# Performance work log

Hardware: AMD Instinct MI355X
Metric: run time of the kernel (lower is better)

## Reference

```python
import jax, jax.numpy as jnp
import numpy as np

N = 50000        # nodes
E = 400000       # edges (avg degree 8)
T = 4            # edge types
D_IN = 64        # input feature dim
D_OUT = 128      # GGNN hidden / output dim
B = 64           # graphs in batch
STEPS = 8        # GRU propagation steps


def setup_inputs() -> dict:
    key = jax.random.key(0)
    ks = jax.random.split(key, 10)
    s = 1.0 / np.sqrt(D_OUT)
    features = jax.random.normal(ks[0], (N, D_IN), jnp.float32)
    src = jax.random.randint(ks[1], (E,), 0, N, jnp.int32)
    dst = jax.random.randint(ks[2], (E,), 0, N, jnp.int32)
    etype = jax.random.randint(ks[3], (E,), 0, T, jnp.int32)
    node2graph = jnp.sort(jax.random.randint(ks[4], (N,), 0, B, jnp.int32))
    # per-edge-type message Linear(out, out)
    W_msg = jax.random.normal(ks[5], (T, D_OUT, D_OUT), jnp.float32) * s
    b_msg = jnp.zeros((T, D_OUT), jnp.float32)
    # GRUCell(out, out): gate order (r, z, n) as in torch
    w_ih = jax.random.normal(ks[6], (D_OUT, 3 * D_OUT), jnp.float32) * s
    b_ih = jnp.zeros((3 * D_OUT,), jnp.float32)
    w_hh = jax.random.normal(ks[7], (D_OUT, 3 * D_OUT), jnp.float32) * s
    b_hh = jnp.zeros((3 * D_OUT,), jnp.float32)
    # classifier Linear(out, 2)
    W_cls = jax.random.normal(ks[8], (D_OUT, 2), jnp.float32) * s
    b_cls = jnp.zeros((2,), jnp.float32)
    return {"features": features, "src": src, "dst": dst, "etype": etype,
            "node2graph": node2graph, "W_msg": W_msg, "b_msg": b_msg,
            "w_ih": w_ih, "b_ih": b_ih, "w_hh": w_hh, "b_hh": b_hh,
            "W_cls": W_cls, "b_cls": b_cls}


def reference(features, src, dst, etype, node2graph, W_msg, b_msg,
              w_ih, b_ih, w_hh, b_hh, W_cls, b_cls):
    n = features.shape[0]
    # zero-pad input features to D_OUT (as in GGNN.forward)
    h1 = jnp.concatenate(
        [features, jnp.zeros((n, D_OUT - D_IN), features.dtype)], axis=-1)

    def step(h, _):
        # transform every node by every etype weight: [N, T, D]
        t = jnp.einsum('nd,tde->nte', h, W_msg) + b_msg
        msgs = t[src, etype]                       # [E, D] gather per edge
        a = jax.ops.segment_sum(msgs, dst, num_segments=n)  # scatter-sum
        # torch GRUCell(a, h), gates ordered (r, z, n)
        gi = a @ w_ih + b_ih
        gh = h @ w_hh + b_hh
        i_r, i_z, i_n = jnp.split(gi, 3, axis=-1)
        h_r, h_z, h_n = jnp.split(gh, 3, axis=-1)
        r = jax.nn.sigmoid(i_r + h_r)
        z = jax.nn.sigmoid(i_z + h_z)
        ng = jnp.tanh(i_n + r * h_n)
        return (1.0 - z) * ng + z * h, None

    h, _ = jax.lax.scan(step, h1, None, length=STEPS)
    hres = h + h1                                   # residual as in forward
    # read_out == 'sum': per-graph segment sum (dgl.sum_nodes)
    feats_g = jax.ops.segment_sum(hres, node2graph, num_segments=B)  # [B, D]
    return feats_g @ W_cls + b_cls                  # [B, 2]
```

## Files before the change

kernel.cpp:

```cpp
#include <hip/hip_runtime.h>
#include <hip/hip_bf16.h>
#include <math.h>

#define NN 50000
#define EE 400000
#define TT 4
#define DIN 64
#define DD 128
#define BB 64
#define STEPS 8
#define KAGG 544
#define KTOT 672
#define NGATES 512
#define NBIN (4 * NN)
#define NBLK ((NBIN + 255) / 256)
#define MT64 ((NN + 63) / 64)

typedef __attribute__((ext_vector_type(8))) short bf16x8;
typedef __attribute__((ext_vector_type(4))) float f32x4;
typedef __attribute__((address_space(3))) void lds_void;
typedef __attribute__((address_space(1))) void glob_void;

__device__ inline float bf2f(__hip_bfloat16 x) { return __bfloat162float(x); }

__device__ inline float s2f(short s) {
    unsigned int u = ((unsigned int)(unsigned short)s) << 16;
    float f;
    __builtin_memcpy(&f, &u, 4);
    return f;
}

__global__ void k_init_h(const float* __restrict__ feat, float* __restrict__ h1,
                         __hip_bfloat16* __restrict__ hb) {
    int idx = blockIdx.x * blockDim.x + threadIdx.x;
    if (idx >= NN * DD) return;
    int v = idx >> 7, d = idx & 127;
    float val = (d < DIN) ? feat[v * DIN + d] : 0.0f;
    h1[idx] = val;
    hb[idx] = __float2bfloat16(val);
}

__global__ void k_zero_i32(int* __restrict__ p, int n) {
    int idx = blockIdx.x * blockDim.x + threadIdx.x;
    if (idx < n) p[idx] = 0;
}
__global__ void k_zero_f32(float* __restrict__ p, int n) {
    int idx = blockIdx.x * blockDim.x + threadIdx.x;
    if (idx < n) p[idx] = 0.0f;
}

__global__ void k_hist(const int* __restrict__ dst, const int* __restrict__ etype,
                       int* __restrict__ deg2) {
    int e = blockIdx.x * blockDim.x + threadIdx.x;
    if (e < EE) atomicAdd(&deg2[dst[e] * 4 + etype[e]], 1);
}

__global__ __launch_bounds__(256) void k_scan_bsum(const int* __restrict__ deg2,
                                                   int* __restrict__ bsum) {
    __shared__ int red[256];
    int tid = threadIdx.x;
    int i = blockIdx.x * 256 + tid;
    int v = (i < NBIN) ? deg2[i] : 0;
    red[tid] = v;
    __syncthreads();
#pragma unroll
    for (int s = 128; s > 0; s >>= 1) {
        if (tid < s) red[tid] += red[tid + s];
        __syncthreads();
    }
    if (tid == 0) bsum[blockIdx.x] = red[0];
}

__global__ __launch_bounds__(1024) void k_scan_boff(const int* __restrict__ bsum,
                                                    int* __restrict__ boff) {
    __shared__ int s[1024];
    int tid = threadIdx.x;
    int v = (tid < NBLK) ? bsum[tid] : 0;
    s[tid] = v;
    __syncthreads();
    for (int d = 1; d < 1024; d <<= 1) {
        int t = (tid >= d) ? s[tid - d] : 0;
        __syncthreads();
        s[tid] += t;
        __syncthreads();
    }
    if (tid < NBLK) boff[tid] = s[tid] - v;
}

__global__ __launch_bounds__(256) void k_scan_final(const int* __restrict__ deg2,
                                                    const int* __restrict__ boff,
                                                    int* __restrict__ off2,
                                                    int* __restrict__ cursor) {
    __shared__ int s[256];
    int tid = threadIdx.x;
    int i = blockIdx.x * 256 + tid;
    int v = (i < NBIN) ? deg2[i] : 0;
    s[tid] = v;
    __syncthreads();
#pragma unroll
    for (int d = 1; d < 256; d <<= 1) {
        int t = (tid >= d) ? s[tid - d] : 0;
        __syncthreads();
        s[tid] += t;
        __syncthreads();
    }
    int excl = boff[blockIdx.x] + s[tid] - v;
    if (i < NBIN) {
        off2[i] = excl;
        cursor[i] = excl;
        if (i == NBIN - 1) off2[NBIN] = excl + v;
    }
}

__global__ void k_fill(const int* __restrict__ dst, const int* __restrict__ src,
                       const int* __restrict__ etype, int* __restrict__ cursor,
                       int* __restrict__ csr_src) {
    int e = blockIdx.x * blockDim.x + threadIdx.x;
    if (e < EE) {
        int pos = atomicAdd(&cursor[dst[e] * 4 + etype[e]], 1);
        csr_src[pos] = src[e];
    }
}

__global__ void k_counts(const int* __restrict__ off2, __hip_bfloat16* __restrict__ g) {
    int idx = blockIdx.x * blockDim.x + threadIdx.x;
    if (idx >= NN * 16) return;
    int v = idx >> 4, j = idx & 15;
    float x = 0.0f, y = 0.0f;
    if (j < 2) {
        int t0 = 2 * j;
        x = (float)(off2[4 * v + t0 + 1] - off2[4 * v + t0]);
        y = (float)(off2[4 * v + t0 + 2] - off2[4 * v + t0 + 1]);
    }
    __hip_bfloat162 o;
    o.x = __float2bfloat16(x);
    o.y = __float2bfloat16(y);
    ((__hip_bfloat162*)(g + (size_t)v * KAGG))[256 + j] = o;
}

__global__ void k_prep2(const float* __restrict__ Wm, const float* __restrict__ bm,
                        const float* __restrict__ wih, const float* __restrict__ whh,
                        const float* __restrict__ bih, const float* __restrict__ bhh,
                        __hip_bfloat16* __restrict__ W2, float* __restrict__ bias512) {
    int idx = blockIdx.x * blockDim.x + threadIdx.x;
    if (idx < 512 * KTOT) {
        int n = idx / KTOT, k = idx % KTOT;
        float v = 0.0f;
        if (k < 544) {
            if (n < 384 && k < 516) {
                float s = 0.0f;
                if (k < 512) {
                    int t = k >> 7, d = k & 127;
                    const float* wr = Wm + (t << 14) + (d << 7);
#pragma unroll 4
                    for (int e = 0; e < 128; ++e) s += wr[e] * wih[e * 384 + n];
                } else {
                    const float* br = bm + ((k - 512) << 7);
#pragma unroll 4
                    for (int e = 0; e < 128; ++e) s += br[e] * wih[e * 384 + n];
                }
                v = s;
            }
        } else {
            int dd = k - 544;
            if (n < 256) v = whh[dd * 384 + n];
            else if (n >= 384) v = whh[dd * 384 + n - 128];
        }
        W2[idx] = __float2bfloat16(v);
    } else {
        int b = idx - 512 * KTOT;
        if (b < NGATES) {
            float v;
            if (b < 256) v = bih[b] + bhh[b];
            else if (b < 384) v = bih[b];
            else v = bhh[b - 128];
            bias512[b] = v;
        }
    }
}

__global__ __launch_bounds__(256) void k_agg(const __hip_bfloat16* __restrict__ hb,
                                             const int* __restrict__ off2,
                                             const int* __restrict__ csr_src,
                                             __hip_bfloat16* __restrict__ g) {
    const int node = (blockIdx.x * blockDim.x + threadIdx.x) >> 6;
    const int lane = threadIdx.x & 63;
    if (node >= NN) return;
    const int t = lane >> 4;
    const int sub = lane & 15;
    const int p0 = off2[4 * node + t];
    const int p1 = off2[4 * node + t + 1];
    float a[8];
#pragma unroll
    for (int j = 0; j < 8; ++j) a[j] = 0.0f;
    int p = p0;
    for (; p + 1 < p1; p += 2) {
        int s0 = csr_src[p];
        int s1 = csr_src[p + 1];
        bf16x8 v0 = *(const bf16x8*)(hb + (size_t)s0 * DD + sub * 8);
        bf16x8 v1 = *(const bf16x8*)(hb + (size_t)s1 * DD + sub * 8);
#pragma unroll
        for (int j = 0; j < 8; ++j) a[j] += s2f(v0[j]) + s2f(v1[j]);
    }
    if (p < p1) {
        int s0 = csr_src[p];
        bf16x8 v0 = *(const bf16x8*)(hb + (size_t)s0 * DD + sub * 8);
#pragma unroll
        for (int j = 0; j < 8; ++j) a[j] += s2f(v0[j]);
    }
    bf16x8 o;
#pragma unroll
    for (int j = 0; j < 8; ++j) {
        __hip_bfloat16 b = __float2bfloat16(a[j]);
        o[j] = *(short*)&b;
    }
    *(bf16x8*)(g + (size_t)node * KAGG + t * 128 + sub * 8) = o;
}

__global__ __launch_bounds__(512, 4) void k_step(const __hip_bfloat16* __restrict__ g,
                                                 const __hip_bfloat16* __restrict__ W2,
                                                 const float* __restrict__ bias512,
                                                 const __hip_bfloat16* __restrict__ hbi,
                                                 __hip_bfloat16* __restrict__ hbo) {
    __shared__ __align__(16) short As[4][64 * 32];
    __shared__ __align__(16) short Bs[2][384 * 32];
    const int tid = threadIdx.x;
    const int lane = tid & 63;
    const int wave = tid >> 6;
    const int row0 = blockIdx.x * 64;
    const int quad = lane >> 4;
    const int m16 = lane & 15;
    const int koff = ((quad ^ ((m16 ^ (m16 >> 2)) & 3)) << 3);
    const int brb = wave * 16 + m16;

    const int arow = tid >> 2;
    const int apart = (tid & 3) ^ ((arow ^ (arow >> 2)) & 3);
    int agrow = row0 + arow;
    if (agrow >= NN) agrow = NN - 1;
    const __hip_bfloat16* gA = g + (size_t)agrow * KAGG + apart * 8;
    const __hip_bfloat16* hA = hbi + (size_t)agrow * DD + apart * 8;

    auto stage_A = [&](int kc) {
        if (wave < 4) {
            const glob_void* srcA = (kc < 17)
                                        ? (const glob_void*)(gA + kc * 32)
                                        : (const glob_void*)(hA + (kc - 17) * 32);
            __builtin_amdgcn_global_load_lds(srcA, (lds_void*)&As[kc & 3][(wave * 64) * 8],
                                             16, 0, 0);
        }
    };
    auto stage_B = [&](int kc) {
#pragma unroll
        for (int i = 0; i < 3; ++i) {
            int s = tid + i * 512;
            int br = s >> 2;
            int bpart = (s & 3) ^ ((br ^ (br >> 2)) & 3);
            int grp = br >> 7;
            int within = br & 127;
            size_t n;
            int kk;
            if (kc < 17) {
                n = (size_t)(grp * 128 + within);
                kk = kc * 32 + bpart * 8;
            } else {
                n = (size_t)((grp < 2 ? grp * 128 : 384) + within);
                kk = 544 + (kc - 17) * 32 + bpart * 8;
            }
            __builtin_amdgcn_global_load_lds((const glob_void*)(W2 + n * KTOT + kk),
                                             (lds_void*)&Bs[kc & 1][(wave * 64 + i * 512) * 8],
                                             16, 0, 0);
        }
    };

    f32x4 acc[4][4];
#pragma unroll
    for (int rt = 0; rt < 4; ++rt)
#pragma unroll
        for (int c = 0; c < 4; ++c) acc[rt][c] = (f32x4){0.f, 0.f, 0.f, 0.f};

    stage_B(0);
    stage_A(0);
    stage_A(1);
    stage_A(2);

    for (int ki = 0; ki < 21; ++ki) {
        if (wave < 4) {
            if (ki == 0)
                asm volatile("s_waitcnt vmcnt(2)" ::: "memory");
            else if (ki <= 18)
                asm volatile("s_waitcnt vmcnt(1)" ::: "memory");
            else
                asm volatile("s_waitcnt vmcnt(0)" ::: "memory");
        } else {
            asm volatile("s_waitcnt vmcnt(0)" ::: "memory");
        }
        __builtin_amdgcn_s_barrier();
        asm volatile("" ::: "memory");
        __builtin_amdgcn_sched_barrier(0);

        if (ki + 1 < 21) stage_B(ki + 1);
        if (ki + 3 < 21) stage_A(ki + 3);

        bf16x8 af[4];
#pragma unroll
        for (int rt = 0; rt < 4; ++rt)
            af[rt] = *(const bf16x8*)&As[ki & 3][(rt * 16 + m16) * 32 + koff];
        bf16x8 b0 = *(const bf16x8*)&Bs[ki & 1][(brb)*32 + koff];
        bf16x8 b1 = *(const bf16x8*)&Bs[ki & 1][(128 + brb) * 32 + koff];
        bf16x8 b2 = *(const bf16x8*)&Bs[ki & 1][(256 + brb) * 32 + koff];
#pragma unroll
        for (int rt = 0; rt < 4; ++rt)
            acc[rt][0] = __builtin_amdgcn_mfma_f32_16x16x32_bf16(af[rt], b0, acc[rt][0], 0, 0, 0);
#pragma unroll
        for (int rt = 0; rt < 4; ++rt)
            acc[rt][1] = __builtin_amdgcn_mfma_f32_16x16x32_bf16(af[rt], b1, acc[rt][1], 0, 0, 0);
        if (ki < 17) {
#pragma unroll
            for (int rt = 0; rt < 4; ++rt)
                acc[rt][2] = __builtin_amdgcn_mfma_f32_16x16x32_bf16(af[rt], b2, acc[rt][2], 0, 0, 0);
        } else {
#pragma unroll
            for (int rt = 0; rt < 4; ++rt)
                acc[rt][3] = __builtin_amdgcn_mfma_f32_16x16x32_bf16(af[rt], b2, acc[rt][3], 0, 0, 0);
        }
    }
    __syncthreads();

    short* Ht = &Bs[0][0];
    {
        const int d = wave * 16 + m16;
        const float brs = bias512[d];
        const float bzs = bias512[128 + d];
        const float bin_ = bias512[256 + d];
        const float bhn = bias512[384 + d];
#pragma unroll
        for (int rt = 0; rt < 4; ++rt) {
#pragma unroll
            for (int j = 0; j < 4; ++j) {
                const int rowl = rt * 16 + quad * 4 + j;
                const int grow = row0 + rowl;
                const float rs = acc[rt][0][j] + brs;
                const float zs = acc[rt][1][j] + bzs;
                const float inn = acc[rt][2][j] + bin_;
                const float hnn = acc[rt][3][j] + bhn;
                const float rr = 1.0f / (1.0f + __expf(-rs));
                const float zz = 1.0f / (1.0f + __expf(-zs));
                const float ng = tanhf(inn + rr * hnn);
                const float hv =
                    bf2f(hbi[(size_t)(grow < NN ? grow : NN - 1) * DD + d]);
                const float o = (1.0f - zz) * ng + zz * hv;
                __hip_bfloat16 ob = __float2bfloat16(o);
                Ht[rowl * 128 + d] = *(short*)&ob;
            }
        }
    }
    __syncthreads();
    {
        const int row = tid >> 3;
        const int col = (tid & 7) * 16;
        if (row0 + row < NN) {
            bf16x8 v0 = *(const bf16x8*)&Ht[row * 128 + col];
            bf16x8 v1 = *(const bf16x8*)&Ht[row * 128 + col + 8];
            __hip_bfloat16* dstp = hbo + (size_t)(row0 + row) * DD + col;
            *(bf16x8*)dstp = v0;
            *(bf16x8*)(dstp + 8) = v1;
        }
    }
}

__global__ __launch_bounds__(128) void k_readout(const __hip_bfloat16* __restrict__ h,
                                                 const float* __restrict__ h1,
                                                 const int* __restrict__ n2g,
                                                 float* __restrict__ feats) {
    const int CHN = 64;
    int d = threadIdx.x;
    int v0 = blockIdx.x * CHN;
    if (v0 >= NN) return;
    int v1 = v0 + CHN;
    if (v1 > NN) v1 = NN;
    float sum = 0.0f;
    int cur = n2g[v0];
    for (int v = v0; v < v1; ++v) {
        int gph = n2g[v];
        if (gph != cur) {
            atomicAdd(&feats[cur * DD + d], sum);
            sum = 0.0f;
            cur = gph;
        }
        sum += bf2f(h[(size_t)v * DD + d]) + h1[(size_t)v * DD + d];
    }
    atomicAdd(&feats[cur * DD + d], sum);
}

__global__ void k_cls(const float* __restrict__ feats, const float* __restrict__ Wc,
                      const float* __restrict__ bc, float* __restrict__ out) {
    int t = threadIdx.x;
    if (t >= BB * 2) return;
    int b = t >> 1, c = t & 1;
    float s = bc[c];
    for (int d = 0; d < DD; ++d) s += feats[b * DD + d] * Wc[d * 2 + c];
    out[t] = s;
}

extern "C" void kernel_launch(void* const* d_in, const int* in_sizes, int n_in, void* d_out,
                              int out_size, void* d_ws, size_t ws_size, hipStream_t stream) {
    const float* features = (const float*)d_in[0];
    const int* src = (const int*)d_in[1];
    const int* dst = (const int*)d_in[2];
    const int* etype = (const int*)d_in[3];
    const int* n2g = (const int*)d_in[4];
    const float* W_msg = (const float*)d_in[5];
    const float* b_msg = (const float*)d_in[6];
    const float* w_ih = (const float*)d_in[7];
    const float* b_ih = (const float*)d_in[8];
    const float* w_hh = (const float*)d_in[9];
    const float* b_hh = (const float*)d_in[10];
    const float* W_cls = (const float*)d_in[11];
    const float* b_cls = (const float*)d_in[12];
    float* out = (float*)d_out;

    char* ws = (char*)d_ws;
    size_t o = 0;
    auto alloc = [&](size_t bytes) {
        o = (o + 255) & ~(size_t)255;
        void* p = ws + o;
        o += bytes;
        return p;
    };
    int* deg2 = (int*)alloc(sizeof(int) * NBIN);
    int* off2 = (int*)alloc(sizeof(int) * (NBIN + 1));
    int* cursor = (int*)alloc(sizeof(int) * NBIN);
    int* bsum = (int*)alloc(sizeof(int) * NBLK);
    int* boff = (int*)alloc(sizeof(int) * NBLK);
    int* csr_src = (int*)alloc(sizeof(int) * EE);
    __hip_bfloat16* W2 = (__hip_bfloat16*)alloc(sizeof(__hip_bfloat16) * 512 * KTOT);
    float* bias512 = (float*)alloc(sizeof(float) * NGATES);
    float* hini = (float*)alloc(sizeof(float) * (size_t)NN * DD);
    __hip_bfloat16* hbfA = (__hip_bfloat16*)alloc(sizeof(__hip_bfloat16) * (size_t)NN * DD);
    __hip_bfloat16* hbfB = (__hip_bfloat16*)alloc(sizeof(__hip_bfloat16) * (size_t)NN * DD);
    __hip_bfloat16* g = (__hip_bfloat16*)alloc(sizeof(__hip_bfloat16) * (size_t)NN * KAGG);
    float* feats = (float*)alloc(sizeof(float) * BB * DD);

    k_init_h<<<(NN * DD + 255) / 256, 256, 0, stream>>>(features, hini, hbfA);
    k_zero_i32<<<(NBIN + 255) / 256, 256, 0, stream>>>(deg2, NBIN);
    k_zero_f32<<<(BB * DD + 255) / 256, 256, 0, stream>>>(feats, BB * DD);
    k_hist<<<(EE + 255) / 256, 256, 0, stream>>>(dst, etype, deg2);
    k_scan_bsum<<<NBLK, 256, 0, stream>>>(deg2, bsum);
    k_scan_boff<<<1, 1024, 0, stream>>>(bsum, boff);
    k_scan_final<<<NBLK, 256, 0, stream>>>(deg2, boff, off2, cursor);
    k_fill<<<(EE + 255) / 256, 256, 0, stream>>>(dst, src, etype, cursor, csr_src);
    k_counts<<<(NN * 16 + 255) / 256, 256, 0, stream>>>(off2, g);
    {
        int prep_n = 512 * KTOT + NGATES;
        k_prep2<<<(prep_n + 255) / 256, 256, 0, stream>>>(W_msg, b_msg, w_ih, w_hh, b_ih,
                                                          b_hh, W2, bias512);
    }

    __hip_bfloat16* hbc = hbfA;
    __hip_bfloat16* hbx = hbfB;
    for (int s = 0; s < STEPS; ++s) {
        k_agg<<<(NN * 64 + 255) / 256, 256, 0, stream>>>(hbc, off2, csr_src, g);
        k_step<<<MT64, 512, 0, stream>>>(g, W2, bias512, hbc, hbx);
        __hip_bfloat16* tb = hbc; hbc = hbx; hbx = tb;
    }
    k_readout<<<(NN + 63) / 64, 128, 0, stream>>>(hbc, hini, n2g, feats);
    k_cls<<<1, 128, 0, stream>>>(feats, W_cls, b_cls, out);
}
```

Baseline: 880.7 us.

## Prepack weights in MFMA fragment order and load operands directly from global

The combined weight matrix is now prepacked into a per-k-chunk, per-wave, per-lane fragment layout. Each wave then reads its B fragments with one coalesced 16-byte load per lane, and A fragments are read straight from global memory, so the LDS staging, async global-to-LDS copies and per-chunk barriers are gone. LDS use shrinks to a small padded output tile, which may allow more blocks per CU. The cost is that every wave reloads the A rows redundantly from global or L2, and global latency is no longer hidden by an explicit multi-stage pipeline.

```diff
diff --git a/kernel.cpp b/kernel.cpp
--- a/kernel.cpp
+++ b/kernel.cpp
@@ -10,16 +10,14 @@
 #define BB 64
 #define STEPS 8
 #define KAGG 544
-#define KTOT 672
 #define NGATES 512
 #define NBIN (4 * NN)
 #define NBLK ((NBIN + 255) / 256)
 #define MT64 ((NN + 63) / 64)
+#define W2F_N (21 * 12288)
 
 typedef __attribute__((ext_vector_type(8))) short bf16x8;
 typedef __attribute__((ext_vector_type(4))) float f32x4;
-typedef __attribute__((address_space(3))) void lds_void;
-typedef __attribute__((address_space(1))) void glob_void;
 
 __device__ inline float bf2f(__hip_bfloat16 x) { return __bfloat162float(x); }
 
@@ -138,44 +136,56 @@
     ((__hip_bfloat162*)(g + (size_t)v * KAGG))[256 + j] = o;
 }
 
-__global__ void k_prep2(const float* __restrict__ Wm, const float* __restrict__ bm,
-                        const float* __restrict__ wih, const float* __restrict__ whh,
-                        const float* __restrict__ bih, const float* __restrict__ bhh,
-                        __hip_bfloat16* __restrict__ W2, float* __restrict__ bias512) {
+__global__ void k_prep_w2f(const float* __restrict__ Wm, const float* __restrict__ bm,
+                           const float* __restrict__ wih, const float* __restrict__ whh,
+                           const float* __restrict__ bih, const float* __restrict__ bhh,
+                           __hip_bfloat16* __restrict__ W2f, float* __restrict__ bias512) {
     int idx = blockIdx.x * blockDim.x + threadIdx.x;
-    if (idx < 512 * KTOT) {
-        int n = idx / KTOT, k = idx % KTOT;
+    if (idx < W2F_N) {
+        int kc = idx / 12288;
+        int r1 = idx % 12288;
+        int gb = r1 >> 12;
+        int r2 = r1 & 4095;
+        int w = r2 >> 9;
+        int r3 = r2 & 511;
+        int l = r3 >> 3;
+        int j = r3 & 7;
+        int npart = w * 16 + (l & 15);
+        int kin = ((l >> 4) << 3) + j;
         float v = 0.0f;
-        if (k < 544) {
-            if (n < 384 && k < 516) {
+        if (kc < 17) {
+            int k = kc * 32 + kin;
+            int n = gb * 128 + npart;
+            if (k < 512) {
+                int t = k >> 7, kd = k & 127;
+                const float* wr = Wm + (t << 14) + (kd << 7);
                 float s = 0.0f;
-                if (k < 512) {
-                    int t = k >> 7, d = k & 127;
-                    const float* wr = Wm + (t << 14) + (d << 7);
 #pragma unroll 4
-                    for (int e = 0; e < 128; ++e) s += wr[e] * wih[e * 384 + n];
-                } else {
-                    const float* br = bm + ((k - 512) << 7);
+                for (int e = 0; e < 128; ++e) s += wr[e] * wih[e * 384 + n];
+                v = s;
+            } else if (k < 516) {
+                const float* br = bm + ((k - 512) << 7);
+                float s = 0.0f;
 #pragma unroll 4
-                    for (int e = 0; e < 128; ++e) s += br[e] * wih[e * 384 + n];
-                }
+                for (int e = 0; e < 128; ++e) s += br[e] * wih[e * 384 + n];
                 v = s;
             }
         } else {
-            int dd = k - 544;
-            if (n < 256) v = whh[dd * 384 + n];
-            else if (n >= 384) v = whh[dd * 384 + n - 128];
+            int kh = (kc - 17) * 32 + kin;
+            int nlog = (gb < 2) ? gb * 128 + npart : 384 + npart;
+            int col = (nlog < 256) ? nlog : nlog - 128;
+            v = whh[kh * 384 + col];
         }
-        W2[idx] = __float2bfloat16(v);
-    } else {
-        int b = idx - 512 * KTOT;
-        if (b < NGATES) {
-            float v;
-            if (b < 256) v = bih[b] + bhh[b];
-            else if (b < 384) v = bih[b];
-            else v = bhh[b - 128];
-            bias512[b] = v;
-        }
+        W2f[idx] = __float2bfloat16(v);
+        return;
+    }
+    int b = idx - W2F_N;
+    if (b < NGATES) {
+        float v;
+        if (b < 256) v = bih[b] + bhh[b];
+        else if (b < 384) v = bih[b];
+        else v = bhh[b - 128];
+        bias512[b] = v;
     }
 }
 
@@ -218,59 +228,28 @@
 }
 
 __global__ __launch_bounds__(512, 4) void k_step(const __hip_bfloat16* __restrict__ g,
-                                                 const __hip_bfloat16* __restrict__ W2,
+                                                 const __hip_bfloat16* __restrict__ W2f,
                                                  const float* __restrict__ bias512,
                                                  const __hip_bfloat16* __restrict__ hbi,
                                                  __hip_bfloat16* __restrict__ hbo) {
-    __shared__ __align__(16) short As[4][64 * 32];
-    __shared__ __align__(16) short Bs[2][384 * 32];
+    __shared__ short Ht[64 * 132];
     const int tid = threadIdx.x;
     const int lane = tid & 63;
     const int wave = tid >> 6;
     const int row0 = blockIdx.x * 64;
     const int quad = lane >> 4;
     const int m16 = lane & 15;
-    const int koff = ((quad ^ ((m16 ^ (m16 >> 2)) & 3)) << 3);
-    const int brb = wave * 16 + m16;
-
-    const int arow = tid >> 2;
-    const int apart = (tid & 3) ^ ((arow ^ (arow >> 2)) & 3);
-    int agrow = row0 + arow;
-    if (agrow >= NN) agrow = NN - 1;
-    const __hip_bfloat16* gA = g + (size_t)agrow * KAGG + apart * 8;
-    const __hip_bfloat16* hA = hbi + (size_t)agrow * DD + apart * 8;
-
-    auto stage_A = [&](int kc) {
-        if (wave < 4) {
-            const glob_void* srcA = (kc < 17)
-                                        ? (const glob_void*)(gA + kc * 32)
-                                        : (const glob_void*)(hA + (kc - 17) * 32);
-            __builtin_amdgcn_global_load_lds(srcA, (lds_void*)&As[kc & 3][(wave * 64) * 8],
-                                             16, 0, 0);
-        }
-    };
-    auto stage_B = [&](int kc) {
-#pragma unroll
-        for (int i = 0; i < 3; ++i) {
-            int s = tid + i * 512;
-            int br = s >> 2;
-            int bpart = (s & 3) ^ ((br ^ (br >> 2)) & 3);
-            int grp = br >> 7;
-            int within = br & 127;
-            size_t n;
-            int kk;
-            if (kc < 17) {
-                n = (size_t)(grp * 128 + within);
-                kk = kc * 32 + bpart * 8;
-            } else {
-                n = (size_t)((grp < 2 ? grp * 128 : 384) + within);
-                kk = 544 + (kc - 17) * 32 + bpart * 8;
-            }
-            __builtin_amdgcn_global_load_lds((const glob_void*)(W2 + n * KTOT + kk),
-                                             (lds_void*)&Bs[kc & 1][(wave * 64 + i * 512) * 8],
-                                             16, 0, 0);
-        }
-    };
+
+    const __hip_bfloat16* ga[4];
+    const __hip_bfloat16* ha[4];
+#pragma unroll
+    for (int rt = 0; rt < 4; ++rt) {
+        int r = row0 + rt * 16 + m16;
+        if (r >= NN) r = NN - 1;
+        ga[rt] = g + (size_t)r * KAGG + quad * 8;
+        ha[rt] = hbi + (size_t)r * DD + quad * 8;
+    }
+    const __hip_bfloat16* bw = W2f + ((wave * 64 + lane) << 3);
 
     f32x4 acc[4][4];
 #pragma unroll
@@ -278,55 +257,46 @@
 #pragma unroll
         for (int c = 0; c < 4; ++c) acc[rt][c] = (f32x4){0.f, 0.f, 0.f, 0.f};
 
-    stage_B(0);
-    stage_A(0);
-    stage_A(1);
-    stage_A(2);
-
-    for (int ki = 0; ki < 21; ++ki) {
-        if (wave < 4) {
-            if (ki == 0)
-                asm volatile("s_waitcnt vmcnt(2)" ::: "memory");
-            else if (ki <= 18)
-                asm volatile("s_waitcnt vmcnt(1)" ::: "memory");
-            else
-                asm volatile("s_waitcnt vmcnt(0)" ::: "memory");
-        } else {
-            asm volatile("s_waitcnt vmcnt(0)" ::: "memory");
-        }
-        __builtin_amdgcn_s_barrier();
-        asm volatile("" ::: "memory");
-        __builtin_amdgcn_sched_barrier(0);
-
-        if (ki + 1 < 21) stage_B(ki + 1);
-        if (ki + 3 < 21) stage_A(ki + 3);
-
+#pragma unroll
+    for (int kc = 0; kc < 17; ++kc) {
         bf16x8 af[4];
 #pragma unroll
-        for (int rt = 0; rt < 4; ++rt)
-            af[rt] = *(const bf16x8*)&As[ki & 3][(rt * 16 + m16) * 32 + koff];
-        bf16x8 b0 = *(const bf16x8*)&Bs[ki & 1][(brb)*32 + koff];
-        bf16x8 b1 = *(const bf16x8*)&Bs[ki & 1][(128 + brb) * 32 + koff];
-        bf16x8 b2 = *(const bf16x8*)&Bs[ki & 1][(256 + brb) * 32 + koff];
+        for (int rt = 0; rt < 4; ++rt) af[rt] = *(const bf16x8*)(ga[rt] + kc * 32);
+        const __hip_bfloat16* bp = bw + kc * 12288;
+        bf16x8 b0 = *(const bf16x8*)(bp);
+        bf16x8 b1 = *(const bf16x8*)(bp + 4096);
+        bf16x8 b2 = *(const bf16x8*)(bp + 8192);
 #pragma unroll
         for (int rt = 0; rt < 4; ++rt)
             acc[rt][0] = __builtin_amdgcn_mfma_f32_16x16x32_bf16(af[rt], b0, acc[rt][0], 0, 0, 0);
 #pragma unroll
         for (int rt = 0; rt < 4; ++rt)
             acc[rt][1] = __builtin_amdgcn_mfma_f32_16x16x32_bf16(af[rt], b1, acc[rt][1], 0, 0, 0);
-        if (ki < 17) {
-#pragma unroll
-            for (int rt = 0; rt < 4; ++rt)
-                acc[rt][2] = __builtin_amdgcn_mfma_f32_16x16x32_bf16(af[rt], b2, acc[rt][2], 0, 0, 0);
-        } else {
-#pragma unroll
-            for (int rt = 0; rt < 4; ++rt)
-                acc[rt][3] = __builtin_amdgcn_mfma_f32_16x16x32_bf16(af[rt], b2, acc[rt][3], 0, 0, 0);
-        }
-    }
-    __syncthreads();
-
-    short* Ht = &Bs[0][0];
+#pragma unroll
+        for (int rt = 0; rt < 4; ++rt)
+            acc[rt][2] = __builtin_amdgcn_mfma_f32_16x16x32_bf16(af[rt], b2, acc[rt][2], 0, 0, 0);
+    }
+#pragma unroll
+    for (int kc = 17; kc < 21; ++kc) {
+        bf16x8 af[4];
+#pragma unroll
+        for (int rt = 0; rt < 4; ++rt)
+            af[rt] = *(const bf16x8*)(ha[rt] + (kc - 17) * 32);
+        const __hip_bfloat16* bp = bw + kc * 12288;
+        bf16x8 b0 = *(const bf16x8*)(bp);
+        bf16x8 b1 = *(const bf16x8*)(bp + 4096);
+        bf16x8 b2 = *(const bf16x8*)(bp + 8192);
+#pragma unroll
+        for (int rt = 0; rt < 4; ++rt)
+            acc[rt][0] = __builtin_amdgcn_mfma_f32_16x16x32_bf16(af[rt], b0, acc[rt][0], 0, 0, 0);
+#pragma unroll
+        for (int rt = 0; rt < 4; ++rt)
+            acc[rt][1] = __builtin_amdgcn_mfma_f32_16x16x32_bf16(af[rt], b1, acc[rt][1], 0, 0, 0);
+#pragma unroll
+        for (int rt = 0; rt < 4; ++rt)
+            acc[rt][3] = __builtin_amdgcn_mfma_f32_16x16x32_bf16(af[rt], b2, acc[rt][3], 0, 0, 0);
+    }
+
     {
         const int d = wave * 16 + m16;
         const float brs = bias512[d];
@@ -350,7 +320,7 @@
                     bf2f(hbi[(size_t)(grow < NN ? grow : NN - 1) * DD + d]);
                 const float o = (1.0f - zz) * ng + zz * hv;
                 __hip_bfloat16 ob = __float2bfloat16(o);
-                Ht[rowl * 128 + d] = *(short*)&ob;
+                Ht[rowl * 132 + d] = *(short*)&ob;
             }
         }
     }
@@ -359,8 +329,8 @@
         const int row = tid >> 3;
         const int col = (tid & 7) * 16;
         if (row0 + row < NN) {
-            bf16x8 v0 = *(const bf16x8*)&Ht[row * 128 + col];
-            bf16x8 v1 = *(const bf16x8*)&Ht[row * 128 + col + 8];
+            bf16x8 v0 = *(const bf16x8*)&Ht[row * 132 + col];
+            bf16x8 v1 = *(const bf16x8*)&Ht[row * 132 + col + 8];
             __hip_bfloat16* dstp = hbo + (size_t)(row0 + row) * DD + col;
             *(bf16x8*)dstp = v0;
             *(bf16x8*)(dstp + 8) = v1;
@@ -433,7 +403,7 @@
     int* bsum = (int*)alloc(sizeof(int) * NBLK);
     int* boff = (int*)alloc(sizeof(int) * NBLK);
     int* csr_src = (int*)alloc(sizeof(int) * EE);
-    __hip_bfloat16* W2 = (__hip_bfloat16*)alloc(sizeof(__hip_bfloat16) * 512 * KTOT);
+    __hip_bfloat16* W2f = (__hip_bfloat16*)alloc(sizeof(__hip_bfloat16) * W2F_N);
     float* bias512 = (float*)alloc(sizeof(float) * NGATES);
     float* hini = (float*)alloc(sizeof(float) * (size_t)NN * DD);
     __hip_bfloat16* hbfA = (__hip_bfloat16*)alloc(sizeof(__hip_bfloat16) * (size_t)NN * DD);
@@ -451,16 +421,16 @@
     k_fill<<<(EE + 255) / 256, 256, 0, stream>>>(dst, src, etype, cursor, csr_src);
     k_counts<<<(NN * 16 + 255) / 256, 256, 0, stream>>>(off2, g);
     {
-        int prep_n = 512 * KTOT + NGATES;
-        k_prep2<<<(prep_n + 255) / 256, 256, 0, stream>>>(W_msg, b_msg, w_ih, w_hh, b_ih,
-                                                          b_hh, W2, bias512);
+        int prep_n = W2F_N + NGATES;
+        k_prep_w2f<<<(prep_n + 255) / 256, 256, 0, stream>>>(W_msg, b_msg, w_ih, w_hh,
+                                                             b_ih, b_hh, W2f, bias512);
     }
 
     __hip_bfloat16* hbc = hbfA;
     __hip_bfloat16* hbx = hbfB;
     for (int s = 0; s < STEPS; ++s) {
         k_agg<<<(NN * 64 + 255) / 256, 256, 0, stream>>>(hbc, off2, csr_src, g);
-        k_step<<<MT64, 512, 0, stream>>>(g, W2, bias512, hbc, hbx);
+        k_step<<<MT64, 512, 0, stream>>>(g, W2f, bias512, hbc, hbx);
         __hip_bfloat16* tb = hbc; hbc = hbx; hbx = tb;
     }
     k_readout<<<(NN + 63) / 64, 128, 0, stream>>>(hbc, hini, n2g, feats);
```

Result: slower. 959.9 us (+9.0%).
